# Optimization experiments

Measured on AMD Instinct MI355X. Metric: run time of the kernel, lower is better.

The kernel has to match this reference:

```python
import jax, jax.numpy as jnp
import numpy as np

# Fixed production-scale dims (equal-size graphs -> no ragged padding needed)
B, NPG, C, H, L, FFN, NC = 16, 512, 128, 8, 4, 512, 4
D = C // H          # head dim = 16
T = NPG + 1         # +1 virtual graph token
EPG = 8192          # edges per graph (avg degree 16)
E = B * EPG


def _ln(x, g, b, eps=1e-5):
    m = x.mean(-1, keepdims=True)
    v = ((x - m) ** 2).mean(-1, keepdims=True)
    return (x - m) * jax.lax.rsqrt(v + eps) * g + b


def setup_inputs() -> dict:
    key = jax.random.key(0)
    ks = jax.random.split(key, 24)
    N = B * NPG
    node_feats = jax.random.normal(ks[0], (N, 3), jnp.float32)
    # intra-graph edges: local endpoints + per-graph node offset (matches batch_ptr math)
    local = jax.random.randint(ks[1], (2, B, EPG), 0, NPG)
    offs = (jnp.arange(B) * NPG)[None, :, None]
    edge_index = (local + offs).reshape(2, E)
    edge_attr = jax.random.randint(ks[2], (E,), 0, 10)

    def nrm(k, shape, scale=0.02):
        return jax.random.normal(k, shape, jnp.float32) * scale

    params = {
        "W_node": nrm(ks[3], (3, C), 0.3), "b_node": jnp.zeros((C,), jnp.float32),
        "graph_token": nrm(ks[4], (C,), 1.0),
        "edge_bias_table": nrm(ks[5], (11, H), 0.1).at[0].set(0.0),  # padding_idx=0
        "in_deg_emb": nrm(ks[6], (512, C)).at[0].set(0.0),           # padding_idx=0
        "out_deg_emb": nrm(ks[7], (512, C)).at[0].set(0.0),
        "vnode_bias": nrm(ks[8], (H,), 1.0),
        "Wq": nrm(ks[9], (L, C, C)), "bq": jnp.zeros((L, C), jnp.float32),
        "Wk": nrm(ks[10], (L, C, C)), "bk": jnp.zeros((L, C), jnp.float32),
        "Wv": nrm(ks[11], (L, C, C)), "bv": jnp.zeros((L, C), jnp.float32),
        "Wo": nrm(ks[12], (L, C, C)), "bo": jnp.zeros((L, C), jnp.float32),
        "ln1_g": jnp.ones((L, C), jnp.float32), "ln1_b": jnp.zeros((L, C), jnp.float32),
        "ln2_g": jnp.ones((L, C), jnp.float32), "ln2_b": jnp.zeros((L, C), jnp.float32),
        "W1": nrm(ks[13], (L, C, FFN)), "b1": jnp.zeros((L, FFN), jnp.float32),
        "W2": nrm(ks[14], (L, FFN, C)), "b2": jnp.zeros((L, C), jnp.float32),
        "normf_g": jnp.ones((C,), jnp.float32), "normf_b": jnp.zeros((C,), jnp.float32),
        "Wc1": nrm(ks[15], (C, C // 2)), "bc1": jnp.zeros((C // 2,), jnp.float32),
        "Wc2": nrm(ks[16], (C // 2, NC)), "bc2": jnp.zeros((NC,), jnp.float32),
    }
    return {"node_feats": node_feats, "edge_index": edge_index,
            "edge_attr": edge_attr, "num_graphs": B, **params}


def reference(node_feats, W_node, b_node, graph_token, edge_bias_table,
              in_deg_emb, out_deg_emb, vnode_bias,
              Wq, bq, Wk, bk, Wv, bv, Wo, bo,
              ln1_g, ln1_b, ln2_g, ln2_b, W1, b1, W2, b2,
              normf_g, normf_b, Wc1, bc1, Wc2, bc2,
              edge_index, edge_attr, num_graphs):
    N = node_feats.shape[0]
    npg = N // num_graphs
    t = npg + 1
    src, dst = edge_index[0], edge_index[1]
    # degree encoders (scatter_add of ones == segment_sum)
    in_deg = jnp.clip(jax.ops.segment_sum(jnp.ones_like(dst), dst, num_segments=N), 0, 511)
    out_deg = jnp.clip(jax.ops.segment_sum(jnp.ones_like(src), src, num_segments=N), 0, 511)
    x_enc = node_feats @ W_node + b_node + in_deg_emb[in_deg] + out_deg_emb[out_deg]
    # equal-size graphs with sorted batch ids -> padding loop is a reshape, mask all-False
    x = jnp.concatenate(
        [jnp.broadcast_to(graph_token, (num_graphs, 1, C)),
         x_enc.reshape(num_graphs, npg, C)], axis=1)  # [B, T, C]
    # attention bias: vnode row/col + scattered edge-attr embeddings
    bias = jnp.zeros((num_graphs, H, t, t), jnp.float32)
    bias = bias.at[:, :, 0, :].set(vnode_bias[None, :, None])
    bias = bias.at[:, :, :, 0].set(vnode_bias[None, :, None])
    eb = edge_bias_table[jnp.clip(edge_attr, 0, 9) + 1]  # [E, H]
    g = src // npg
    sl = src - g * npg + 1
    dl = dst - g * npg + 1
    bias = bias.at[g, :, sl, dl].add(eb)  # duplicate edges accumulate (scatter_add)
    scale = 1.0 / np.sqrt(D).astype(np.float32)
    for l in range(L):  # key_padding_mask is all-False here -> masked_fill is a no-op
        h = _ln(x, ln1_g[l], ln1_b[l])
        q = (h @ Wq[l] + bq[l]).reshape(num_graphs, t, H, D)
        k = (h @ Wk[l] + bk[l]).reshape(num_graphs, t, H, D)
        v = (h @ Wv[l] + bv[l]).reshape(num_graphs, t, H, D)
        scores = jnp.einsum('bthd,bshd->bhts', q, k) * scale + bias
        attn = jax.nn.softmax(scores, axis=-1)
        o = jnp.einsum('bhts,bshd->bthd', attn, v).reshape(num_graphs, t, C)
        x = x + o @ Wo[l] + bo[l]
        h2 = _ln(x, ln2_g[l], ln2_b[l])
        x = x + jax.nn.gelu(h2 @ W1[l] + b1[l], approximate=False) @ W2[l] + b2[l]
    x = _ln(x, normf_g, normf_b)
    gr = x[:, 0, :]  # virtual-node readout
    return jax.nn.gelu(gr @ Wc1 + bc1, approximate=False) @ Wc2 + bc2
```

## Files before the change

kernel.cpp:

```cpp
#include <hip/hip_runtime.h>
#include <hip/hip_bf16.h>

#define BB 16
#define NPG 512
#define CC 128
#define HH 8
#define LL 4
#define FFN 512
#define NCLS 4
#define DD 16
#define TT 513
#define EE 131072
#define NNODES 8192
#define ROWS (BB * TT)
#define ECAP 64
#define SP 544
#define BSTR 292

static constexpr size_t XROWS = (size_t)BB * TT;
static constexpr size_t XSZ   = XROWS * CC;
static constexpr size_t VTSZ  = (size_t)BB * HH * DD * SP;

typedef unsigned short ushort_t;
typedef __attribute__((ext_vector_type(8))) short short8;
typedef __attribute__((ext_vector_type(4))) float floatx4;

__device__ __forceinline__ float gelu_exact(float v) {
    return 0.5f * v * (1.0f + erff(v * 0.70710678118654752440f));
}
__device__ __forceinline__ ushort_t f2bf(float f) {
    union { float f; unsigned u; } c; c.f = f;
    unsigned u = c.u;
    return (ushort_t)((u + 0x7FFFu + ((u >> 16) & 1u)) >> 16);
}
__device__ __forceinline__ int swz(int row, int col, int stride) {
    int kb = col >> 3;
    return row * stride + (((kb ^ (row & 7)) << 3) | (col & 7));
}

__device__ __forceinline__ void qkv_stage(const ushort_t* hs,
                                          const ushort_t* Wtq, const float* bq_,
                                          const ushort_t* Wtk, const float* bk_,
                                          const ushort_t* Wtv, const float* bv_,
                                          ushort_t* qb, ushort_t* kb, ushort_t* vt,
                                          int m0, int wave, int lq, int quad) {
    const short* hsS = (const short*)hs;
    int n0 = wave * 32;
    int c0 = n0 + lq, c1 = n0 + 16 + lq;
    const short* Ws[3] = {(const short*)Wtq, (const short*)Wtk, (const short*)Wtv};
    const float* bs[3] = {bq_, bk_, bv_};
    size_t rB0 = (size_t)(n0 + lq) * CC, rB1 = (size_t)(n0 + 16 + lq) * CC;

    #pragma unroll
    for (int m = 0; m < 3; ++m) {
        const short* W = Ws[m];
        floatx4 a0 = {0.f,0.f,0.f,0.f}, a1 = a0;
        #pragma unroll
        for (int k0 = 0; k0 < CC; k0 += 32) {
            short8 af = *(const short8*)(hsS + swz(lq, k0 + quad * 8, 128));
            short8 b0 = *(const short8*)(W + rB0 + k0 + quad * 8);
            short8 b1 = *(const short8*)(W + rB1 + k0 + quad * 8);
            a0 = __builtin_amdgcn_mfma_f32_16x16x32_bf16(af, b0, a0, 0, 0, 0);
            a1 = __builtin_amdgcn_mfma_f32_16x16x32_bf16(af, b1, a1, 0, 0, 0);
        }
        float bv0 = bs[m][c0], bv1 = bs[m][c1];
        #pragma unroll
        for (int rg = 0; rg < 4; ++rg) {
            int r = m0 + quad * 4 + rg;
            float v0 = a0[rg] + bv0;
            float v1 = a1[rg] + bv1;
            if (m == 0) {
                qb[(size_t)r * CC + c0] = f2bf(v0 * 0.25f);
                qb[(size_t)r * CC + c1] = f2bf(v1 * 0.25f);
            } else if (m == 1) {
                kb[(size_t)r * CC + c0] = f2bf(v0);
                kb[(size_t)r * CC + c1] = f2bf(v1);
            } else {
                int bg = r / TT;
                int s = r - bg * TT;
                vt[((size_t)(bg * HH + (c0 >> 4)) * DD + (c0 & 15)) * SP + s] = f2bf(v0);
                vt[((size_t)(bg * HH + (c1 >> 4)) * DD + (c1 & 15)) * SP + s] = f2bf(v1);
            }
        }
    }
}

__global__ __launch_bounds__(256) void deg_csr_kernel(const int* __restrict__ ei,
                                                      const int* __restrict__ ea,
                                                      int* __restrict__ deg_in,
                                                      int* __restrict__ deg_out,
                                                      int* __restrict__ cnt,
                                                      int* __restrict__ ebuf) {
    int e = blockIdx.x * 256 + threadIdx.x;
    if (e >= EE) return;
    int src = ei[e], dst = ei[EE + e];
    atomicAdd(&deg_out[src], 1);
    atomicAdd(&deg_in[dst], 1);
    int g = src >> 9;
    int sl = src - (g << 9) + 1;
    int dl = dst - (g << 9) + 1;
    int a = ea[e];
    a = (a < 0) ? 0 : (a > 9 ? 9 : a);
    a += 1;
    int row = g * TT + sl;
    int pos = atomicAdd(&cnt[row], 1);
    if (pos < ECAP) ebuf[(size_t)row * ECAP + pos] = dl | (a << 16);
}

__global__ __launch_bounds__(256) void encode_kernel(const float* __restrict__ nf,
                                                     const float* __restrict__ Wn,
                                                     const float* __restrict__ bn,
                                                     const float* __restrict__ gt,
                                                     const float* __restrict__ ide,
                                                     const float* __restrict__ ode,
                                                     const int* __restrict__ deg_in,
                                                     const int* __restrict__ deg_out,
                                                     float* __restrict__ x) {
    int gid = blockIdx.x * 256 + threadIdx.x;
    if (gid >= (int)(XROWS * CC)) return;
    int c = gid & (CC - 1);
    int row = gid >> 7;
    int b = row / TT;
    int t = row - b * TT;
    float val;
    if (t == 0) {
        val = gt[c];
    } else {
        int i = b * NPG + t - 1;
        val = bn[c] + nf[i*3+0]*Wn[0*CC + c] + nf[i*3+1]*Wn[1*CC + c] + nf[i*3+2]*Wn[2*CC + c];
        int di = min(deg_in[i], 511);
        int dq = min(deg_out[i], 511);
        val += ide[(size_t)di * CC + c] + ode[(size_t)dq * CC + c];
    }
    x[(size_t)row * CC + c] = val;
}

struct TrDesc {
    const float* src[24];
    ushort_t*    dst[24];
    int          K[24];
    int          N[24];
};
__global__ __launch_bounds__(256) void tr_kernel(TrDesc d) {
    int z = blockIdx.z;
    int K = d.K[z], N = d.N[z];
    int tilesN = N >> 6;
    int ntile = (K >> 6) * tilesN;
    int tile = blockIdx.x;
    if (tile >= ntile) return;
    int k0 = (tile / tilesN) << 6;
    int n0 = (tile - (tile / tilesN) * tilesN) << 6;
    const float* src = d.src[z];
    ushort_t* dst = d.dst[z];
    __shared__ float t[64][65];
    int tid = threadIdx.x;
    int c = tid & 63, rb = tid >> 6;
    #pragma unroll
    for (int kk = 0; kk < 64; kk += 4)
        t[kk + rb][c] = src[(size_t)(k0 + kk + rb) * N + n0 + c];
    __syncthreads();
    #pragma unroll
    for (int nn = 0; nn < 64; nn += 4)
        dst[(size_t)(n0 + nn + rb) * K + k0 + c] = f2bf(t[c][nn + rb]);
}

__global__ __launch_bounds__(256) void pre_kernel(const float* __restrict__ x_,
                                                  const float* __restrict__ ln1g_,
                                                  const float* __restrict__ ln1b_,
                                                  const ushort_t* __restrict__ Wtq,
                                                  const float* __restrict__ bq_,
                                                  const ushort_t* __restrict__ Wtk,
                                                  const float* __restrict__ bk_,
                                                  const ushort_t* __restrict__ Wtv,
                                                  const float* __restrict__ bv_,
                                                  ushort_t* __restrict__ qb,
                                                  ushort_t* __restrict__ kb,
                                                  ushort_t* __restrict__ vt) {
    int m0 = blockIdx.x * 16;
    int tid = threadIdx.x;
    int wave = tid >> 6, lane = tid & 63, lq = lane & 15, quad = lane >> 4;

    __shared__ ushort_t hs[16 * 128];
    __shared__ float sred[4][16][2];

    int n0 = wave * 32;
    int c0 = n0 + lq, c1 = n0 + 16 + lq;
    float w0[4], w1[4];
    #pragma unroll
    for (int rg = 0; rg < 4; ++rg) {
        int r = m0 + quad * 4 + rg;
        w0[rg] = x_[(size_t)r * CC + c0];
        w1[rg] = x_[(size_t)r * CC + c1];
    }
    #pragma unroll
    for (int rg = 0; rg < 4; ++rg) {
        float s1 = w0[rg] + w1[rg];
        float s2 = w0[rg]*w0[rg] + w1[rg]*w1[rg];
        #pragma unroll
        for (int m = 1; m < 16; m <<= 1) {
            s1 += __shfl_xor(s1, m, 64);
            s2 += __shfl_xor(s2, m, 64);
        }
        if (lq == 0) { sred[wave][quad*4+rg][0] = s1; sred[wave][quad*4+rg][1] = s2; }
    }
    __syncthreads();
    float g0 = ln1g_[c0], g1 = ln1g_[c1], lb0 = ln1b_[c0], lb1 = ln1b_[c1];
    #pragma unroll
    for (int rg = 0; rg < 4; ++rg) {
        int row = quad * 4 + rg;
        float S1 = sred[0][row][0] + sred[1][row][0] + sred[2][row][0] + sred[3][row][0];
        float S2 = sred[0][row][1] + sred[1][row][1] + sred[2][row][1] + sred[3][row][1];
        float mn = S1 * (1.0f/CC);
        float var = S2 * (1.0f/CC) - mn * mn;
        float rs = rsqrtf(var + 1e-5f);
        hs[swz(row, c0, 128)] = f2bf((w0[rg] - mn) * rs * g0 + lb0);
        hs[swz(row, c1, 128)] = f2bf((w1[rg] - mn) * rs * g1 + lb1);
    }
    __syncthreads();
    qkv_stage(hs, Wtq, bq_, Wtk, bk_, Wtv, bv_, qb, kb, vt, m0, wave, lq, quad);
}

__global__ __launch_bounds__(256) void mega_kernel(const ushort_t* __restrict__ obf,
                                                   const ushort_t* __restrict__ WtO,
                                                   const float* __restrict__ bo_,
                                                   const float* __restrict__ ln2g_,
                                                   const float* __restrict__ ln2b_,
                                                   const ushort_t* __restrict__ Wt1_,
                                                   const float* __restrict__ b1_,
                                                   const ushort_t* __restrict__ Wt2_,
                                                   const float* __restrict__ b2_,
                                                   const float* __restrict__ ln1g_,
                                                   const float* __restrict__ ln1b_,
                                                   const ushort_t* __restrict__ Wtq,
                                                   const float* __restrict__ bq_,
                                                   const ushort_t* __restrict__ Wtk,
                                                   const float* __restrict__ bk_,
                                                   const ushort_t* __restrict__ Wtv,
                                                   const float* __restrict__ bv_,
                                                   float* __restrict__ x_,
                                                   ushort_t* __restrict__ qb,
                                                   ushort_t* __restrict__ kb,
                                                   ushort_t* __restrict__ vt,
                                                   int doQKV) {
    int m0 = blockIdx.x * 16;
    int tid = threadIdx.x;
    int wave = tid >> 6, lane = tid & 63, lq = lane & 15, quad = lane >> 4;

    __shared__ ushort_t hs[16 * 128];
    __shared__ ushort_t ms[16 * 512];
    __shared__ float sred[4][16][2];

    int n0 = wave * 32;
    int c0 = n0 + lq, c1 = n0 + 16 + lq;
    float vv0[4], vv1[4];

    {
        const short* Ab = (const short*)obf;
        const short* W = (const short*)WtO;
        size_t rowA = (size_t)(m0 + lq) * CC;
        size_t rB0 = (size_t)(n0 + lq) * CC, rB1 = (size_t)(n0 + 16 + lq) * CC;
        floatx4 a0 = {0.f,0.f,0.f,0.f}, a1 = a0;
        #pragma unroll
        for (int k0 = 0; k0 < CC; k0 += 32) {
            short8 af = *(const short8*)(Ab + rowA + k0 + quad * 8);
            short8 b0 = *(const short8*)(W + rB0 + k0 + quad * 8);
            short8 b1 = *(const short8*)(W + rB1 + k0 + quad * 8);
            a0 = __builtin_amdgcn_mfma_f32_16x16x32_bf16(af, b0, a0, 0, 0, 0);
            a1 = __builtin_amdgcn_mfma_f32_16x16x32_bf16(af, b1, a1, 0, 0, 0);
        }
        float bv0 = bo_[c0], bv1 = bo_[c1];
        #pragma unroll
        for (int rg = 0; rg < 4; ++rg) {
            int r = m0 + quad * 4 + rg;
            vv0[rg] = a0[rg] + bv0 + x_[(size_t)r * CC + c0];
            vv1[rg] = a1[rg] + bv1 + x_[(size_t)r * CC + c1];
        }
        #pragma unroll
        for (int rg = 0; rg < 4; ++rg) {
            float s1 = vv0[rg] + vv1[rg];
            float s2 = vv0[rg]*vv0[rg] + vv1[rg]*vv1[rg];
            #pragma unroll
            for (int m = 1; m < 16; m <<= 1) {
                s1 += __shfl_xor(s1, m, 64);
                s2 += __shfl_xor(s2, m, 64);
            }
            if (lq == 0) { sred[wave][quad*4+rg][0] = s1; sred[wave][quad*4+rg][1] = s2; }
        }
        __syncthreads();
        float g0 = ln2g_[c0], g1 = ln2g_[c1], lb0 = ln2b_[c0], lb1 = ln2b_[c1];
        #pragma unroll
        for (int rg = 0; rg < 4; ++rg) {
            int row = quad * 4 + rg;
            float S1 = sred[0][row][0] + sred[1][row][0] + sred[2][row][0] + sred[3][row][0];
            float S2 = sred[0][row][1] + sred[1][row][1] + sred[2][row][1] + sred[3][row][1];
            float mn = S1 * (1.0f/CC);
            float var = S2 * (1.0f/CC) - mn * mn;
            float rs = rsqrtf(var + 1e-5f);
            hs[swz(row, c0, 128)] = f2bf((vv0[rg] - mn) * rs * g0 + lb0);
            hs[swz(row, c1, 128)] = f2bf((vv1[rg] - mn) * rs * g1 + lb1);
        }
    }
    __syncthreads();

    {
        const short* hsS = (const short*)hs;
        const short* W = (const short*)Wt1_;
        #pragma unroll
        for (int nt = 0; nt < 4; ++nt) {
            int n = wave * 128 + nt * 32;
            size_t rB0 = (size_t)(n + lq) * CC, rB1 = (size_t)(n + 16 + lq) * CC;
            floatx4 a0 = {0.f,0.f,0.f,0.f}, a1 = a0;
            #pragma unroll
            for (int k0 = 0; k0 < CC; k0 += 32) {
                short8 af = *(const short8*)(hsS + swz(lq, k0 + quad * 8, 128));
                short8 b0 = *(const short8*)(W + rB0 + k0 + quad * 8);
                short8 b1 = *(const short8*)(W + rB1 + k0 + quad * 8);
                a0 = __builtin_amdgcn_mfma_f32_16x16x32_bf16(af, b0, a0, 0, 0, 0);
                a1 = __builtin_amdgcn_mfma_f32_16x16x32_bf16(af, b1, a1, 0, 0, 0);
            }
            float bb0 = b1_[n + lq], bb1 = b1_[n + 16 + lq];
            #pragma unroll
            for (int rg = 0; rg < 4; ++rg) {
                int row = quad * 4 + rg;
                ms[swz(row, n + lq, 512)]      = f2bf(gelu_exact(a0[rg] + bb0));
                ms[swz(row, n + 16 + lq, 512)] = f2bf(gelu_exact(a1[rg] + bb1));
            }
        }
    }
    __syncthreads();

    {
        const short* msS = (const short*)ms;
        const short* W = (const short*)Wt2_;
        size_t rB0 = (size_t)(n0 + lq) * FFN, rB1 = (size_t)(n0 + 16 + lq) * FFN;
        floatx4 a0 = {0.f,0.f,0.f,0.f}, a1 = a0;
        #pragma unroll 4
        for (int k0 = 0; k0 < FFN; k0 += 32) {
            short8 af = *(const short8*)(msS + swz(lq, k0 + quad * 8, 512));
            short8 b0 = *(const short8*)(W + rB0 + k0 + quad * 8);
            short8 b1 = *(const short8*)(W + rB1 + k0 + quad * 8);
            a0 = __builtin_amdgcn_mfma_f32_16x16x32_bf16(af, b0, a0, 0, 0, 0);
            a1 = __builtin_amdgcn_mfma_f32_16x16x32_bf16(af, b1, a1, 0, 0, 0);
        }
        float bv0 = b2_[c0], bv1 = b2_[c1];
        float w0[4], w1[4];
        #pragma unroll
        for (int rg = 0; rg < 4; ++rg) {
            int r = m0 + quad * 4 + rg;
            w0[rg] = a0[rg] + bv0 + vv0[rg];
            w1[rg] = a1[rg] + bv1 + vv1[rg];
            x_[(size_t)r * CC + c0] = w0[rg];
            x_[(size_t)r * CC + c1] = w1[rg];
        }
        if (!doQKV) return;
        #pragma unroll
        for (int rg = 0; rg < 4; ++rg) {
            float s1 = w0[rg] + w1[rg];
            float s2 = w0[rg]*w0[rg] + w1[rg]*w1[rg];
            #pragma unroll
            for (int m = 1; m < 16; m <<= 1) {
                s1 += __shfl_xor(s1, m, 64);
                s2 += __shfl_xor(s2, m, 64);
            }
            if (lq == 0) { sred[wave][quad*4+rg][0] = s1; sred[wave][quad*4+rg][1] = s2; }
        }
        __syncthreads();
        float g0 = ln1g_[c0], g1 = ln1g_[c1], lb0 = ln1b_[c0], lb1 = ln1b_[c1];
        #pragma unroll
        for (int rg = 0; rg < 4; ++rg) {
            int row = quad * 4 + rg;
            float S1 = sred[0][row][0] + sred[1][row][0] + sred[2][row][0] + sred[3][row][0];
            float S2 = sred[0][row][1] + sred[1][row][1] + sred[2][row][1] + sred[3][row][1];
            float mn = S1 * (1.0f/CC);
            float var = S2 * (1.0f/CC) - mn * mn;
            float rs = rsqrtf(var + 1e-5f);
            hs[swz(row, c0, 128)] = f2bf((w0[rg] - mn) * rs * g0 + lb0);
            hs[swz(row, c1, 128)] = f2bf((w1[rg] - mn) * rs * g1 + lb1);
        }
    }
    __syncthreads();

    qkv_stage(hs, Wtq, bq_, Wtk, bk_, Wtv, bv_, qb, kb, vt, m0, wave, lq, quad);
}

__global__ __launch_bounds__(256) void attn_kernel(const ushort_t* __restrict__ qb,
                                                   const ushort_t* __restrict__ kb,
                                                   const ushort_t* __restrict__ vt,
                                                   const int* __restrict__ cnt,
                                                   const int* __restrict__ ebuf,
                                                   const float* __restrict__ ebt,
                                                   const float* __restrict__ vnode,
                                                   ushort_t* __restrict__ ob) {
    int bh = blockIdx.x;
    int qt = blockIdx.y;
    int b = bh >> 3, h = bh & (HH - 1);
    int tid = threadIdx.x;
    int wave = tid >> 6, lane = tid & 63, lq = lane & 15, quad = lane >> 4;

    __shared__ float arena[16 * BSTR];
    float* bstrip = arena;

    int qg = qt * 16 + lq;
    int qr = qg < TT ? qg : TT - 1;
    short8 qf = {0,0,0,0,0,0,0,0};
    if (quad < 2)
        qf = *(const short8*)(qb + ((size_t)(b * TT + qr)) * CC + h * DD + quad * 8);
    float vbh = vnode[h];
    int ql = tid >> 4, e0 = tid & 15;
    int qs = qt * 16 + ql;
    int crow = b * TT + (qs < TT ? qs : 0);
    int cn = (qs > 0 && qs < TT) ? min(cnt[crow], ECAP) : 0;

    const short* kbS = (const short*)kb;
    const short* vtS = (const short*)(vt + (size_t)bh * DD * SP);

    floatx4 oacc = {0.f, 0.f, 0.f, 0.f};
    float lsum = 0.f;

    #pragma unroll
    for (int ch = 0; ch < 2; ++ch) {
        int sp_lo = ch ? 9 : 0;
        int sp_hi = ch ? 17 : 9;
        int s_lo  = ch ? 288 : 0;
        int nrows = ch ? 256 : 288;

        int sp = sp_lo + wave;
        short8 af0 = {0,0,0,0,0,0,0,0}, af1 = af0, vf = af0;
        if (sp < sp_hi) {
            int st0 = sp * 2, st1 = sp * 2 + 1;
            int kr0 = min(b * TT + st0 * 16 + lq, (int)XROWS - 1);
            int kr1 = min(b * TT + st1 * 16 + lq, (int)XROWS - 1);
            if (quad < 2) {
                af0 = *(const short8*)(kbS + (size_t)kr0 * CC + h * DD + quad * 8);
                af1 = *(const short8*)(kbS + (size_t)kr1 * CC + h * DD + quad * 8);
            }
            vf = *(const short8*)(vtS + (size_t)lq * SP + sp * 32 + quad * 8);
        }

        for (int i = tid; i < 16 * BSTR / 4; i += 256)
            ((float4*)bstrip)[i] = make_float4(0.f, 0.f, 0.f, 0.f);
        __syncthreads();
        if (ch == 0 && tid < 16) {
            int q = qt * 16 + tid;
            if (q > 0 && q < TT) bstrip[tid * BSTR] = vbh;
        }
        for (int j = e0; j < cn; j += 16) {
            int e = ebuf[(size_t)crow * ECAP + j];
            int dl = e & 0xFFFF, a = e >> 16;
            int loc = dl - s_lo;
            if (loc >= 0 && loc < nrows)
                atomicAdd(&bstrip[ql * BSTR + loc], ebt[a * 8 + h]);
        }
        __syncthreads();

        for (; sp < sp_hi; sp += 4) {
            int spn = sp + 4;
            short8 nf0 = {0,0,0,0,0,0,0,0}, nf1 = nf0, nvf = nf0;
            if (spn < sp_hi) {
                int st0 = spn * 2, st1 = spn * 2 + 1;
                int kr0 = min(b * TT + st0 * 16 + lq, (int)XROWS - 1);
                int kr1 = min(b * TT + st1 * 16 + lq, (int)XROWS - 1);
                if (quad < 2) {
                    nf0 = *(const short8*)(kbS + (size_t)kr0 * CC + h * DD + quad * 8);
                    nf1 = *(const short8*)(kbS + (size_t)kr1 * CC + h * DD + quad * 8);
                }
                nvf = *(const short8*)(vtS + (size_t)lq * SP + spn * 32 + quad * 8);
            }

            unsigned pw[2][2];
            #pragma unroll
            for (int t = 0; t < 2; ++t) {
                int st = sp * 2 + t;
                floatx4 c = __builtin_amdgcn_mfma_f32_16x16x32_bf16(
                    t ? af1 : af0, qf, (floatx4){0.f, 0.f, 0.f, 0.f}, 0, 0, 0);
                float4 bi = *(const float4*)(bstrip + lq * BSTR + (st * 16 - s_lo) + quad * 4);
                float biv[4] = {bi.x, bi.y, bi.z, bi.w};
                float pr[4];
                #pragma unroll
                for (int rg = 0; rg < 4; ++rg) {
                    int s = st * 16 + quad * 4 + rg;
                    float p = 0.f;
                    if (s < TT) p = __expf(c[rg] + biv[rg]);
                    lsum += p;
                    pr[rg] = p;
                }
                pw[t][0] = (unsigned)f2bf(pr[0]) | ((unsigned)f2bf(pr[1]) << 16);
                pw[t][1] = (unsigned)f2bf(pr[2]) | ((unsigned)f2bf(pr[3]) << 16);
            }
            int srcA = lq + (((2 * quad) & 3) << 4);
            int srcB = lq + (((2 * quad + 1) & 3) << 4);
            int a00 = __shfl((int)pw[0][0], srcA, 64);
            int a01 = __shfl((int)pw[0][1], srcA, 64);
            int a10 = __shfl((int)pw[1][0], srcA, 64);
            int a11 = __shfl((int)pw[1][1], srcA, 64);
            int b00 = __shfl((int)pw[0][0], srcB, 64);
            int b01 = __shfl((int)pw[0][1], srcB, 64);
            int b10 = __shfl((int)pw[1][0], srcB, 64);
            int b11 = __shfl((int)pw[1][1], srcB, 64);
            union { int u[4]; short8 s8; } pu;
            bool lo = quad < 2;
            pu.u[0] = lo ? a00 : a10;
            pu.u[1] = lo ? a01 : a11;
            pu.u[2] = lo ? b00 : b10;
            pu.u[3] = lo ? b01 : b11;
            oacc = __builtin_amdgcn_mfma_f32_16x16x32_bf16(vf, pu.s8, oacc, 0, 0, 0);

            af0 = nf0; af1 = nf1; vf = nvf;
        }
        __syncthreads();
    }

    lsum += __shfl_xor(lsum, 16, 64);
    lsum += __shfl_xor(lsum, 32, 64);
    float* redw = arena;
    float* lsumS = arena + 1088;
    #pragma unroll
    for (int rg = 0; rg < 4; ++rg)
        redw[wave * 272 + (quad * 4 + rg) * 17 + lq] = oacc[rg];
    if (quad == 0) lsumS[wave * 16 + lq] = lsum;
    __syncthreads();

    {
        int q = tid >> 4, d = tid & 15;
        float o = 0.f, L = 0.f;
        #pragma unroll
        for (int w = 0; w < 4; ++w) {
            o += redw[w * 272 + d * 17 + q];
            L += lsumS[w * 16 + q];
        }
        int qq = qt * 16 + q;
        if (qq < TT)
            ob[((size_t)(b * TT + qq)) * CC + h * DD + d] = f2bf(o / L);
    }
}

__global__ __launch_bounds__(128) void head_kernel(const float* __restrict__ x,
                                                   const float* __restrict__ ng,
                                                   const float* __restrict__ nb,
                                                   const float* __restrict__ Wc1,
                                                   const float* __restrict__ bc1,
                                                   const float* __restrict__ Wc2,
                                                   const float* __restrict__ bc2,
                                                   float* __restrict__ out) {
    int b = blockIdx.x;
    int c = threadIdx.x;
    __shared__ float xfs[CC];
    __shared__ float c1s[64];
    __shared__ float red[4];

    float v = x[((size_t)b * TT) * CC + c];
    float s1 = v, s2 = v * v;
    #pragma unroll
    for (int m = 32; m >= 1; m >>= 1) {
        s1 += __shfl_xor(s1, m, 64);
        s2 += __shfl_xor(s2, m, 64);
    }
    int w = c >> 6;
    if ((c & 63) == 0) { red[w*2] = s1; red[w*2+1] = s2; }
    __syncthreads();
    float S1 = red[0] + red[2], S2 = red[1] + red[3];
    float mn = S1 * (1.0f/CC);
    float var = S2 * (1.0f/CC) - mn * mn;
    float rs = rsqrtf(var + 1e-5f);
    xfs[c] = (v - mn) * rs * ng[c] + nb[c];
    __syncthreads();
    if (c < 64) {
        float a = bc1[c];
        #pragma unroll 4
        for (int k = 0; k < CC; ++k) a = fmaf(xfs[k], Wc1[(size_t)k * 64 + c], a);
        c1s[c] = gelu_exact(a);
    }
    __syncthreads();
    if (c < NCLS) {
        float a = bc2[c];
        #pragma unroll 4
        for (int j = 0; j < 64; ++j) a = fmaf(c1s[j], Wc2[(size_t)j * NCLS + c], a);
        out[(size_t)b * NCLS + c] = a;
    }
}

extern "C" void kernel_launch(void* const* d_in, const int* in_sizes, int n_in,
                              void* d_out, int out_size, void* d_ws, size_t ws_size,
                              hipStream_t stream) {
    const float* node_feats = (const float*)d_in[0];
    const int*   edge_index = (const int*)d_in[1];
    const int*   edge_attr  = (const int*)d_in[2];
    const float* W_node  = (const float*)d_in[4];
    const float* b_node  = (const float*)d_in[5];
    const float* g_token = (const float*)d_in[6];
    const float* ebt     = (const float*)d_in[7];
    const float* ide     = (const float*)d_in[8];
    const float* ode     = (const float*)d_in[9];
    const float* vnode   = (const float*)d_in[10];
    const float* Wq = (const float*)d_in[11];
    const float* bq = (const float*)d_in[12];
    const float* Wk = (const float*)d_in[13];
    const float* bk = (const float*)d_in[14];
    const float* Wv = (const float*)d_in[15];
    const float* bv = (const float*)d_in[16];
    const float* Wo = (const float*)d_in[17];
    const float* bo = (const float*)d_in[18];
    const float* ln1g = (const float*)d_in[19];
    const float* ln1b = (const float*)d_in[20];
    const float* ln2g = (const float*)d_in[21];
    const float* ln2b = (const float*)d_in[22];
    const float* W1 = (const float*)d_in[23];
    const float* b1 = (const float*)d_in[24];
    const float* W2 = (const float*)d_in[25];
    const float* b2 = (const float*)d_in[26];
    const float* nfg = (const float*)d_in[27];
    const float* nfb = (const float*)d_in[28];
    const float* Wc1 = (const float*)d_in[29];
    const float* bc1 = (const float*)d_in[30];
    const float* Wc2 = (const float*)d_in[31];
    const float* bc2 = (const float*)d_in[32];
    float* out = (float*)d_out;

    char* base = (char*)d_ws;
    float* x      = (float*)base;     base += XSZ * 4;
    ushort_t* qb  = (ushort_t*)base;  base += XSZ * 2;
    ushort_t* kb  = (ushort_t*)base;  base += XSZ * 2;
    ushort_t* vt  = (ushort_t*)base;  base += VTSZ * 2;
    ushort_t* obf = (ushort_t*)base;  base += XSZ * 2;
    ushort_t* wtqkvo = (ushort_t*)base; base += (size_t)16 * 16384 * 2;
    ushort_t* wt1 = (ushort_t*)base;  base += (size_t)4 * 65536 * 2;
    ushort_t* wt2 = (ushort_t*)base;  base += (size_t)4 * 65536 * 2;
    int* deg_in  = (int*)base;        base += NNODES * 4;
    int* deg_out = (int*)base;        base += NNODES * 4;
    int* cnt     = (int*)base;        base += (size_t)ROWS * 4;
    int* ebuf    = (int*)base;        base += (size_t)ROWS * ECAP * 4;

    hipMemsetAsync(deg_in, 0, (size_t)(2 * NNODES + ROWS) * 4, stream);
    deg_csr_kernel<<<EE / 256, 256, 0, stream>>>(edge_index, edge_attr,
                                                 deg_in, deg_out, cnt, ebuf);
    encode_kernel<<<(int)((XROWS * CC + 255) / 256), 256, 0, stream>>>(
        node_feats, W_node, b_node, g_token, ide, ode, deg_in, deg_out, x);

    TrDesc td;
    for (int l = 0; l < LL; ++l) {
        const float* srcs[4] = {Wq + (size_t)l*CC*CC, Wk + (size_t)l*CC*CC,
                                Wv + (size_t)l*CC*CC, Wo + (size_t)l*CC*CC};
        for (int k = 0; k < 4; ++k) {
            int slot = k * 4 + l;
            td.src[slot] = srcs[k];
            td.dst[slot] = wtqkvo + (size_t)slot * 16384;
            td.K[slot] = CC; td.N[slot] = CC;
        }
        td.src[16 + l] = W1 + (size_t)l*CC*FFN;
        td.dst[16 + l] = wt1 + (size_t)l*65536;
        td.K[16 + l] = CC; td.N[16 + l] = FFN;
        td.src[20 + l] = W2 + (size_t)l*FFN*CC;
        td.dst[20 + l] = wt2 + (size_t)l*65536;
        td.K[20 + l] = FFN; td.N[20 + l] = CC;
    }
    tr_kernel<<<dim3(16, 1, 24), 256, 0, stream>>>(td);

    const int MT16 = (int)(XROWS / 16);

    pre_kernel<<<MT16, 256, 0, stream>>>(
        x, ln1g, ln1b,
        wtqkvo + (size_t)(0*4+0)*16384, bq,
        wtqkvo + (size_t)(1*4+0)*16384, bk,
        wtqkvo + (size_t)(2*4+0)*16384, bv,
        qb, kb, vt);

    for (int l = 0; l < LL; ++l) {
        attn_kernel<<<dim3(BB*HH, 33), 256, 0, stream>>>(
            qb, kb, vt, cnt, ebuf, ebt, vnode, obf);

        int ln = (l + 1) % LL;
        mega_kernel<<<MT16, 256, 0, stream>>>(
            obf,
            wtqkvo + (size_t)(3*4+l)*16384, bo + l*CC,
            ln2g + l*CC, ln2b + l*CC,
            wt1 + (size_t)l*65536, b1 + l*FFN,
            wt2 + (size_t)l*65536, b2 + l*CC,
            ln1g + ln*CC, ln1b + ln*CC,
            wtqkvo + (size_t)(0*4+ln)*16384, bq + ln*CC,
            wtqkvo + (size_t)(1*4+ln)*16384, bk + ln*CC,
            wtqkvo + (size_t)(2*4+ln)*16384, bv + ln*CC,
            x, qb, kb, vt,
            (l < LL-1) ? 1 : 0);
    }

    head_kernel<<<BB, 128, 0, stream>>>(x, nfg, nfb, Wc1, bc1, Wc2, bc2, out);
}
```

Measured before the change: 436.0 us.

## Fuse all stages into one persistent cooperative kernel with grid syncs

Replaces the chain of separate kernel launches (degree/CSR build, encode, weight transpose, QKV, per-layer attention and MLP, head) with a single persistent cooperative kernel. Blocks loop over the work of each phase and separate phases with grid-wide syncs. The aim is to remove per-launch overhead and launch gaps. In exchange, the number of resident blocks is capped by occupancy, a shared-memory arena is reused across phases, and grid syncs add their own cost. A multi-launch fallback is kept for when cooperative launch is unavailable.

```diff
diff --git a/kernel.cpp b/kernel.cpp
--- a/kernel.cpp
+++ b/kernel.cpp
@@ -1,5 +1,8 @@
 #include <hip/hip_runtime.h>
 #include <hip/hip_bf16.h>
+#include <hip/hip_cooperative_groups.h>
+
+namespace cg = cooperative_groups;
 
 #define BB 16
 #define NPG 512
@@ -16,6 +19,7 @@
 #define ECAP 64
 #define SP 544
 #define BSTR 292
+#define MT16 513
 
 static constexpr size_t XROWS = (size_t)BB * TT;
 static constexpr size_t XSZ   = XROWS * CC;
@@ -24,6 +28,17 @@
 typedef unsigned short ushort_t;
 typedef __attribute__((ext_vector_type(8))) short short8;
 typedef __attribute__((ext_vector_type(4))) float floatx4;
+
+struct KArgs {
+    const float *node_feats, *W_node, *b_node, *g_token, *ebt, *ide, *ode, *vnode;
+    const float *Wq, *bq, *Wk, *bk, *Wv, *bv, *Wo, *bo;
+    const float *ln1g, *ln1b, *ln2g, *ln2b;
+    const float *W1, *b1, *W2, *b2, *nfg, *nfb, *Wc1, *bc1, *Wc2, *bc2;
+    const int *edge_index, *edge_attr;
+    float *x, *out;
+    ushort_t *qb, *kb, *vt, *obf, *wtqkvo, *wt1, *wt2;
+    int *deg_in, *deg_out, *cnt, *ebuf;
+};
 
 __device__ __forceinline__ float gelu_exact(float v) {
     return 0.5f * v * (1.0f + erff(v * 0.70710678118654752440f));
@@ -38,12 +53,11 @@
     return row * stride + (((kb ^ (row & 7)) << 3) | (col & 7));
 }
 
-__device__ __forceinline__ void qkv_stage(const ushort_t* hs,
-                                          const ushort_t* Wtq, const float* bq_,
-                                          const ushort_t* Wtk, const float* bk_,
-                                          const ushort_t* Wtv, const float* bv_,
-                                          ushort_t* qb, ushort_t* kb, ushort_t* vt,
-                                          int m0, int wave, int lq, int quad) {
+__device__ __forceinline__ void qkv_stage4(const KArgs& a, const ushort_t* hs,
+                                           const ushort_t* Wtq, const float* bq_,
+                                           const ushort_t* Wtk, const float* bk_,
+                                           const ushort_t* Wtv, const float* bv_,
+                                           int m0, int wave, int lq, int quad) {
     const short* hsS = (const short*)hs;
     int n0 = wave * 32;
     int c0 = n0 + lq, c1 = n0 + 16 + lq;
@@ -70,349 +84,39 @@
             float v0 = a0[rg] + bv0;
             float v1 = a1[rg] + bv1;
             if (m == 0) {
-                qb[(size_t)r * CC + c0] = f2bf(v0 * 0.25f);
-                qb[(size_t)r * CC + c1] = f2bf(v1 * 0.25f);
+                a.qb[(size_t)r * CC + c0] = f2bf(v0 * 0.25f);
+                a.qb[(size_t)r * CC + c1] = f2bf(v1 * 0.25f);
             } else if (m == 1) {
-                kb[(size_t)r * CC + c0] = f2bf(v0);
-                kb[(size_t)r * CC + c1] = f2bf(v1);
+                a.kb[(size_t)r * CC + c0] = f2bf(v0);
+                a.kb[(size_t)r * CC + c1] = f2bf(v1);
             } else {
                 int bg = r / TT;
                 int s = r - bg * TT;
-                vt[((size_t)(bg * HH + (c0 >> 4)) * DD + (c0 & 15)) * SP + s] = f2bf(v0);
-                vt[((size_t)(bg * HH + (c1 >> 4)) * DD + (c1 & 15)) * SP + s] = f2bf(v1);
-            }
-        }
-    }
-}
-
-__global__ __launch_bounds__(256) void deg_csr_kernel(const int* __restrict__ ei,
-                                                      const int* __restrict__ ea,
-                                                      int* __restrict__ deg_in,
-                                                      int* __restrict__ deg_out,
-                                                      int* __restrict__ cnt,
-                                                      int* __restrict__ ebuf) {
-    int e = blockIdx.x * 256 + threadIdx.x;
-    if (e >= EE) return;
-    int src = ei[e], dst = ei[EE + e];
-    atomicAdd(&deg_out[src], 1);
-    atomicAdd(&deg_in[dst], 1);
-    int g = src >> 9;
-    int sl = src - (g << 9) + 1;
-    int dl = dst - (g << 9) + 1;
-    int a = ea[e];
-    a = (a < 0) ? 0 : (a > 9 ? 9 : a);
-    a += 1;
-    int row = g * TT + sl;
-    int pos = atomicAdd(&cnt[row], 1);
-    if (pos < ECAP) ebuf[(size_t)row * ECAP + pos] = dl | (a << 16);
-}
-
-__global__ __launch_bounds__(256) void encode_kernel(const float* __restrict__ nf,
-                                                     const float* __restrict__ Wn,
-                                                     const float* __restrict__ bn,
-                                                     const float* __restrict__ gt,
-                                                     const float* __restrict__ ide,
-                                                     const float* __restrict__ ode,
-                                                     const int* __restrict__ deg_in,
-                                                     const int* __restrict__ deg_out,
-                                                     float* __restrict__ x) {
-    int gid = blockIdx.x * 256 + threadIdx.x;
-    if (gid >= (int)(XROWS * CC)) return;
-    int c = gid & (CC - 1);
-    int row = gid >> 7;
-    int b = row / TT;
-    int t = row - b * TT;
-    float val;
-    if (t == 0) {
-        val = gt[c];
-    } else {
-        int i = b * NPG + t - 1;
-        val = bn[c] + nf[i*3+0]*Wn[0*CC + c] + nf[i*3+1]*Wn[1*CC + c] + nf[i*3+2]*Wn[2*CC + c];
-        int di = min(deg_in[i], 511);
-        int dq = min(deg_out[i], 511);
-        val += ide[(size_t)di * CC + c] + ode[(size_t)dq * CC + c];
-    }
-    x[(size_t)row * CC + c] = val;
-}
-
-struct TrDesc {
-    const float* src[24];
-    ushort_t*    dst[24];
-    int          K[24];
-    int          N[24];
-};
-__global__ __launch_bounds__(256) void tr_kernel(TrDesc d) {
-    int z = blockIdx.z;
-    int K = d.K[z], N = d.N[z];
-    int tilesN = N >> 6;
-    int ntile = (K >> 6) * tilesN;
-    int tile = blockIdx.x;
-    if (tile >= ntile) return;
-    int k0 = (tile / tilesN) << 6;
-    int n0 = (tile - (tile / tilesN) * tilesN) << 6;
-    const float* src = d.src[z];
-    ushort_t* dst = d.dst[z];
-    __shared__ float t[64][65];
-    int tid = threadIdx.x;
-    int c = tid & 63, rb = tid >> 6;
-    #pragma unroll
-    for (int kk = 0; kk < 64; kk += 4)
-        t[kk + rb][c] = src[(size_t)(k0 + kk + rb) * N + n0 + c];
-    __syncthreads();
-    #pragma unroll
-    for (int nn = 0; nn < 64; nn += 4)
-        dst[(size_t)(n0 + nn + rb) * K + k0 + c] = f2bf(t[c][nn + rb]);
-}
-
-__global__ __launch_bounds__(256) void pre_kernel(const float* __restrict__ x_,
-                                                  const float* __restrict__ ln1g_,
-                                                  const float* __restrict__ ln1b_,
-                                                  const ushort_t* __restrict__ Wtq,
-                                                  const float* __restrict__ bq_,
-                                                  const ushort_t* __restrict__ Wtk,
-                                                  const float* __restrict__ bk_,
-                                                  const ushort_t* __restrict__ Wtv,
-                                                  const float* __restrict__ bv_,
-                                                  ushort_t* __restrict__ qb,
-                                                  ushort_t* __restrict__ kb,
-                                                  ushort_t* __restrict__ vt) {
-    int m0 = blockIdx.x * 16;
-    int tid = threadIdx.x;
+                a.vt[((size_t)(bg * HH + (c0 >> 4)) * DD + (c0 & 15)) * SP + s] = f2bf(v0);
+                a.vt[((size_t)(bg * HH + (c1 >> 4)) * DD + (c1 & 15)) * SP + s] = f2bf(v1);
+            }
+        }
+    }
+}
+
+__device__ void attn_tile(const KArgs& a, char* arena, int bh, int qt, int tid) {
+    int b = bh >> 3, h = bh & (HH - 1);
     int wave = tid >> 6, lane = tid & 63, lq = lane & 15, quad = lane >> 4;
-
-    __shared__ ushort_t hs[16 * 128];
-    __shared__ float sred[4][16][2];
-
-    int n0 = wave * 32;
-    int c0 = n0 + lq, c1 = n0 + 16 + lq;
-    float w0[4], w1[4];
-    #pragma unroll
-    for (int rg = 0; rg < 4; ++rg) {
-        int r = m0 + quad * 4 + rg;
-        w0[rg] = x_[(size_t)r * CC + c0];
-        w1[rg] = x_[(size_t)r * CC + c1];
-    }
-    #pragma unroll
-    for (int rg = 0; rg < 4; ++rg) {
-        float s1 = w0[rg] + w1[rg];
-        float s2 = w0[rg]*w0[rg] + w1[rg]*w1[rg];
-        #pragma unroll
-        for (int m = 1; m < 16; m <<= 1) {
-            s1 += __shfl_xor(s1, m, 64);
-            s2 += __shfl_xor(s2, m, 64);
-        }
-        if (lq == 0) { sred[wave][quad*4+rg][0] = s1; sred[wave][quad*4+rg][1] = s2; }
-    }
-    __syncthreads();
-    float g0 = ln1g_[c0], g1 = ln1g_[c1], lb0 = ln1b_[c0], lb1 = ln1b_[c1];
-    #pragma unroll
-    for (int rg = 0; rg < 4; ++rg) {
-        int row = quad * 4 + rg;
-        float S1 = sred[0][row][0] + sred[1][row][0] + sred[2][row][0] + sred[3][row][0];
-        float S2 = sred[0][row][1] + sred[1][row][1] + sred[2][row][1] + sred[3][row][1];
-        float mn = S1 * (1.0f/CC);
-        float var = S2 * (1.0f/CC) - mn * mn;
-        float rs = rsqrtf(var + 1e-5f);
-        hs[swz(row, c0, 128)] = f2bf((w0[rg] - mn) * rs * g0 + lb0);
-        hs[swz(row, c1, 128)] = f2bf((w1[rg] - mn) * rs * g1 + lb1);
-    }
-    __syncthreads();
-    qkv_stage(hs, Wtq, bq_, Wtk, bk_, Wtv, bv_, qb, kb, vt, m0, wave, lq, quad);
-}
-
-__global__ __launch_bounds__(256) void mega_kernel(const ushort_t* __restrict__ obf,
-                                                   const ushort_t* __restrict__ WtO,
-                                                   const float* __restrict__ bo_,
-                                                   const float* __restrict__ ln2g_,
-                                                   const float* __restrict__ ln2b_,
-                                                   const ushort_t* __restrict__ Wt1_,
-                                                   const float* __restrict__ b1_,
-                                                   const ushort_t* __restrict__ Wt2_,
-                                                   const float* __restrict__ b2_,
-                                                   const float* __restrict__ ln1g_,
-                                                   const float* __restrict__ ln1b_,
-                                                   const ushort_t* __restrict__ Wtq,
-                                                   const float* __restrict__ bq_,
-                                                   const ushort_t* __restrict__ Wtk,
-                                                   const float* __restrict__ bk_,
-                                                   const ushort_t* __restrict__ Wtv,
-                                                   const float* __restrict__ bv_,
-                                                   float* __restrict__ x_,
-                                                   ushort_t* __restrict__ qb,
-                                                   ushort_t* __restrict__ kb,
-                                                   ushort_t* __restrict__ vt,
-                                                   int doQKV) {
-    int m0 = blockIdx.x * 16;
-    int tid = threadIdx.x;
-    int wave = tid >> 6, lane = tid & 63, lq = lane & 15, quad = lane >> 4;
-
-    __shared__ ushort_t hs[16 * 128];
-    __shared__ ushort_t ms[16 * 512];
-    __shared__ float sred[4][16][2];
-
-    int n0 = wave * 32;
-    int c0 = n0 + lq, c1 = n0 + 16 + lq;
-    float vv0[4], vv1[4];
-
-    {
-        const short* Ab = (const short*)obf;
-        const short* W = (const short*)WtO;
-        size_t rowA = (size_t)(m0 + lq) * CC;
-        size_t rB0 = (size_t)(n0 + lq) * CC, rB1 = (size_t)(n0 + 16 + lq) * CC;
-        floatx4 a0 = {0.f,0.f,0.f,0.f}, a1 = a0;
-        #pragma unroll
-        for (int k0 = 0; k0 < CC; k0 += 32) {
-            short8 af = *(const short8*)(Ab + rowA + k0 + quad * 8);
-            short8 b0 = *(const short8*)(W + rB0 + k0 + quad * 8);
-            short8 b1 = *(const short8*)(W + rB1 + k0 + quad * 8);
-            a0 = __builtin_amdgcn_mfma_f32_16x16x32_bf16(af, b0, a0, 0, 0, 0);
-            a1 = __builtin_amdgcn_mfma_f32_16x16x32_bf16(af, b1, a1, 0, 0, 0);
-        }
-        float bv0 = bo_[c0], bv1 = bo_[c1];
-        #pragma unroll
-        for (int rg = 0; rg < 4; ++rg) {
-            int r = m0 + quad * 4 + rg;
-            vv0[rg] = a0[rg] + bv0 + x_[(size_t)r * CC + c0];
-            vv1[rg] = a1[rg] + bv1 + x_[(size_t)r * CC + c1];
-        }
-        #pragma unroll
-        for (int rg = 0; rg < 4; ++rg) {
-            float s1 = vv0[rg] + vv1[rg];
-            float s2 = vv0[rg]*vv0[rg] + vv1[rg]*vv1[rg];
-            #pragma unroll
-            for (int m = 1; m < 16; m <<= 1) {
-                s1 += __shfl_xor(s1, m, 64);
-                s2 += __shfl_xor(s2, m, 64);
-            }
-            if (lq == 0) { sred[wave][quad*4+rg][0] = s1; sred[wave][quad*4+rg][1] = s2; }
-        }
-        __syncthreads();
-        float g0 = ln2g_[c0], g1 = ln2g_[c1], lb0 = ln2b_[c0], lb1 = ln2b_[c1];
-        #pragma unroll
-        for (int rg = 0; rg < 4; ++rg) {
-            int row = quad * 4 + rg;
-            float S1 = sred[0][row][0] + sred[1][row][0] + sred[2][row][0] + sred[3][row][0];
-            float S2 = sred[0][row][1] + sred[1][row][1] + sred[2][row][1] + sred[3][row][1];
-            float mn = S1 * (1.0f/CC);
-            float var = S2 * (1.0f/CC) - mn * mn;
-            float rs = rsqrtf(var + 1e-5f);
-            hs[swz(row, c0, 128)] = f2bf((vv0[rg] - mn) * rs * g0 + lb0);
-            hs[swz(row, c1, 128)] = f2bf((vv1[rg] - mn) * rs * g1 + lb1);
-        }
-    }
-    __syncthreads();
-
-    {
-        const short* hsS = (const short*)hs;
-        const short* W = (const short*)Wt1_;
-        #pragma unroll
-        for (int nt = 0; nt < 4; ++nt) {
-            int n = wave * 128 + nt * 32;
-            size_t rB0 = (size_t)(n + lq) * CC, rB1 = (size_t)(n + 16 + lq) * CC;
-            floatx4 a0 = {0.f,0.f,0.f,0.f}, a1 = a0;
-            #pragma unroll
-            for (int k0 = 0; k0 < CC; k0 += 32) {
-                short8 af = *(const short8*)(hsS + swz(lq, k0 + quad * 8, 128));
-                short8 b0 = *(const short8*)(W + rB0 + k0 + quad * 8);
-                short8 b1 = *(const short8*)(W + rB1 + k0 + quad * 8);
-                a0 = __builtin_amdgcn_mfma_f32_16x16x32_bf16(af, b0, a0, 0, 0, 0);
-                a1 = __builtin_amdgcn_mfma_f32_16x16x32_bf16(af, b1, a1, 0, 0, 0);
-            }
-            float bb0 = b1_[n + lq], bb1 = b1_[n + 16 + lq];
-            #pragma unroll
-            for (int rg = 0; rg < 4; ++rg) {
-                int row = quad * 4 + rg;
-                ms[swz(row, n + lq, 512)]      = f2bf(gelu_exact(a0[rg] + bb0));
-                ms[swz(row, n + 16 + lq, 512)] = f2bf(gelu_exact(a1[rg] + bb1));
-            }
-        }
-    }
-    __syncthreads();
-
-    {
-        const short* msS = (const short*)ms;
-        const short* W = (const short*)Wt2_;
-        size_t rB0 = (size_t)(n0 + lq) * FFN, rB1 = (size_t)(n0 + 16 + lq) * FFN;
-        floatx4 a0 = {0.f,0.f,0.f,0.f}, a1 = a0;
-        #pragma unroll 4
-        for (int k0 = 0; k0 < FFN; k0 += 32) {
-            short8 af = *(const short8*)(msS + swz(lq, k0 + quad * 8, 512));
-            short8 b0 = *(const short8*)(W + rB0 + k0 + quad * 8);
-            short8 b1 = *(const short8*)(W + rB1 + k0 + quad * 8);
-            a0 = __builtin_amdgcn_mfma_f32_16x16x32_bf16(af, b0, a0, 0, 0, 0);
-            a1 = __builtin_amdgcn_mfma_f32_16x16x32_bf16(af, b1, a1, 0, 0, 0);
-        }
-        float bv0 = b2_[c0], bv1 = b2_[c1];
-        float w0[4], w1[4];
-        #pragma unroll
-        for (int rg = 0; rg < 4; ++rg) {
-            int r = m0 + quad * 4 + rg;
-            w0[rg] = a0[rg] + bv0 + vv0[rg];
-            w1[rg] = a1[rg] + bv1 + vv1[rg];
-            x_[(size_t)r * CC + c0] = w0[rg];
-            x_[(size_t)r * CC + c1] = w1[rg];
-        }
-        if (!doQKV) return;
-        #pragma unroll
-        for (int rg = 0; rg < 4; ++rg) {
-            float s1 = w0[rg] + w1[rg];
-            float s2 = w0[rg]*w0[rg] + w1[rg]*w1[rg];
-            #pragma unroll
-            for (int m = 1; m < 16; m <<= 1) {
-                s1 += __shfl_xor(s1, m, 64);
-                s2 += __shfl_xor(s2, m, 64);
-            }
-            if (lq == 0) { sred[wave][quad*4+rg][0] = s1; sred[wave][quad*4+rg][1] = s2; }
-        }
-        __syncthreads();
-        float g0 = ln1g_[c0], g1 = ln1g_[c1], lb0 = ln1b_[c0], lb1 = ln1b_[c1];
-        #pragma unroll
-        for (int rg = 0; rg < 4; ++rg) {
-            int row = quad * 4 + rg;
-            float S1 = sred[0][row][0] + sred[1][row][0] + sred[2][row][0] + sred[3][row][0];
-            float S2 = sred[0][row][1] + sred[1][row][1] + sred[2][row][1] + sred[3][row][1];
-            float mn = S1 * (1.0f/CC);
-            float var = S2 * (1.0f/CC) - mn * mn;
-            float rs = rsqrtf(var + 1e-5f);
-            hs[swz(row, c0, 128)] = f2bf((w0[rg] - mn) * rs * g0 + lb0);
-            hs[swz(row, c1, 128)] = f2bf((w1[rg] - mn) * rs * g1 + lb1);
-        }
-    }
-    __syncthreads();
-
-    qkv_stage(hs, Wtq, bq_, Wtk, bk_, Wtv, bv_, qb, kb, vt, m0, wave, lq, quad);
-}
-
-__global__ __launch_bounds__(256) void attn_kernel(const ushort_t* __restrict__ qb,
-                                                   const ushort_t* __restrict__ kb,
-                                                   const ushort_t* __restrict__ vt,
-                                                   const int* __restrict__ cnt,
-                                                   const int* __restrict__ ebuf,
-                                                   const float* __restrict__ ebt,
-                                                   const float* __restrict__ vnode,
-                                                   ushort_t* __restrict__ ob) {
-    int bh = blockIdx.x;
-    int qt = blockIdx.y;
-    int b = bh >> 3, h = bh & (HH - 1);
-    int tid = threadIdx.x;
-    int wave = tid >> 6, lane = tid & 63, lq = lane & 15, quad = lane >> 4;
-
-    __shared__ float arena[16 * BSTR];
-    float* bstrip = arena;
+    float* bstrip = (float*)arena;
 
     int qg = qt * 16 + lq;
     int qr = qg < TT ? qg : TT - 1;
     short8 qf = {0,0,0,0,0,0,0,0};
     if (quad < 2)
-        qf = *(const short8*)(qb + ((size_t)(b * TT + qr)) * CC + h * DD + quad * 8);
-    float vbh = vnode[h];
+        qf = *(const short8*)(a.qb + ((size_t)(b * TT + qr)) * CC + h * DD + quad * 8);
+    float vbh = a.vnode[h];
     int ql = tid >> 4, e0 = tid & 15;
     int qs = qt * 16 + ql;
     int crow = b * TT + (qs < TT ? qs : 0);
-    int cn = (qs > 0 && qs < TT) ? min(cnt[crow], ECAP) : 0;
-
-    const short* kbS = (const short*)kb;
-    const short* vtS = (const short*)(vt + (size_t)bh * DD * SP);
+    int cn = (qs > 0 && qs < TT) ? min(a.cnt[crow], ECAP) : 0;
+
+    const short* kbS = (const short*)a.kb;
+    const short* vtS = (const short*)(a.vt + (size_t)bh * DD * SP);
 
     floatx4 oacc = {0.f, 0.f, 0.f, 0.f};
     float lsum = 0.f;
@@ -445,11 +149,11 @@
             if (q > 0 && q < TT) bstrip[tid * BSTR] = vbh;
         }
         for (int j = e0; j < cn; j += 16) {
-            int e = ebuf[(size_t)crow * ECAP + j];
-            int dl = e & 0xFFFF, a = e >> 16;
+            int e = a.ebuf[(size_t)crow * ECAP + j];
+            int dl = e & 0xFFFF, aa = e >> 16;
             int loc = dl - s_lo;
             if (loc >= 0 && loc < nrows)
-                atomicAdd(&bstrip[ql * BSTR + loc], ebt[a * 8 + h]);
+                atomicAdd(&bstrip[ql * BSTR + loc], a.ebt[aa * 8 + h]);
         }
         __syncthreads();
 
@@ -512,8 +216,8 @@
 
     lsum += __shfl_xor(lsum, 16, 64);
     lsum += __shfl_xor(lsum, 32, 64);
-    float* redw = arena;
-    float* lsumS = arena + 1088;
+    float* redw = (float*)arena;
+    float* lsumS = (float*)arena + 1088;
     #pragma unroll
     for (int rg = 0; rg < 4; ++rg)
         redw[wave * 272 + (quad * 4 + rg) * 17 + lq] = oacc[rg];
@@ -530,158 +234,456 @@
         }
         int qq = qt * 16 + q;
         if (qq < TT)
-            ob[((size_t)(b * TT + qq)) * CC + h * DD + d] = f2bf(o / L);
-    }
-}
-
-__global__ __launch_bounds__(128) void head_kernel(const float* __restrict__ x,
-                                                   const float* __restrict__ ng,
-                                                   const float* __restrict__ nb,
-                                                   const float* __restrict__ Wc1,
-                                                   const float* __restrict__ bc1,
-                                                   const float* __restrict__ Wc2,
-                                                   const float* __restrict__ bc2,
-                                                   float* __restrict__ out) {
-    int b = blockIdx.x;
-    int c = threadIdx.x;
-    __shared__ float xfs[CC];
-    __shared__ float c1s[64];
-    __shared__ float red[4];
-
-    float v = x[((size_t)b * TT) * CC + c];
-    float s1 = v, s2 = v * v;
+            a.obf[((size_t)(b * TT + qq)) * CC + h * DD + d] = f2bf(o / L);
+    }
+    __syncthreads();
+}
+
+__device__ void mega_tile(const KArgs& a, char* arena, int l, int m0, int tid, int doQKV) {
+    int wave = tid >> 6, lane = tid & 63, lq = lane & 15, quad = lane >> 4;
+    ushort_t* hs = (ushort_t*)arena;
+    ushort_t* ms = (ushort_t*)(arena + 4096);
+    float* sred = (float*)(arena + 20480);
+
+    const ushort_t* WtO = a.wtqkvo + (size_t)(12 + l) * 16384;
+    const float* bo_ = a.bo + l * CC;
+    const float* ln2g_ = a.ln2g + l * CC;
+    const float* ln2b_ = a.ln2b + l * CC;
+    const ushort_t* Wt1_ = a.wt1 + (size_t)l * 65536;
+    const float* b1_ = a.b1 + l * FFN;
+    const ushort_t* Wt2_ = a.wt2 + (size_t)l * 65536;
+    const float* b2_ = a.b2 + l * CC;
+    int ln = (l + 1) % LL;
+    const float* ln1g_ = a.ln1g + ln * CC;
+    const float* ln1b_ = a.ln1b + ln * CC;
+
+    int n0 = wave * 32;
+    int c0 = n0 + lq, c1 = n0 + 16 + lq;
+    float vv0[4], vv1[4];
+
+    {
+        const short* Ab = (const short*)a.obf;
+        const short* W = (const short*)WtO;
+        size_t rowA = (size_t)(m0 + lq) * CC;
+        size_t rB0 = (size_t)(n0 + lq) * CC, rB1 = (size_t)(n0 + 16 + lq) * CC;
+        floatx4 a0 = {0.f,0.f,0.f,0.f}, a1 = a0;
+        #pragma unroll
+        for (int k0 = 0; k0 < CC; k0 += 32) {
+            short8 af = *(const short8*)(Ab + rowA + k0 + quad * 8);
+            short8 b0 = *(const short8*)(W + rB0 + k0 + quad * 8);
+            short8 b1 = *(const short8*)(W + rB1 + k0 + quad * 8);
+            a0 = __builtin_amdgcn_mfma_f32_16x16x32_bf16(af, b0, a0, 0, 0, 0);
+            a1 = __builtin_amdgcn_mfma_f32_16x16x32_bf16(af, b1, a1, 0, 0, 0);
+        }
+        float bv0 = bo_[c0], bv1 = bo_[c1];
+        #pragma unroll
+        for (int rg = 0; rg < 4; ++rg) {
+            int r = m0 + quad * 4 + rg;
+            vv0[rg] = a0[rg] + bv0 + a.x[(size_t)r * CC + c0];
+            vv1[rg] = a1[rg] + bv1 + a.x[(size_t)r * CC + c1];
+        }
+        #pragma unroll
+        for (int rg = 0; rg < 4; ++rg) {
+            float s1 = vv0[rg] + vv1[rg];
+            float s2 = vv0[rg]*vv0[rg] + vv1[rg]*vv1[rg];
+            #pragma unroll
+            for (int m = 1; m < 16; m <<= 1) {
+                s1 += __shfl_xor(s1, m, 64);
+                s2 += __shfl_xor(s2, m, 64);
+            }
+            if (lq == 0) { sred[(wave*16 + quad*4+rg)*2+0] = s1; sred[(wave*16 + quad*4+rg)*2+1] = s2; }
+        }
+        __syncthreads();
+        float g0 = ln2g_[c0], g1 = ln2g_[c1], lb0 = ln2b_[c0], lb1 = ln2b_[c1];
+        #pragma unroll
+        for (int rg = 0; rg < 4; ++rg) {
+            int row = quad * 4 + rg;
+            float S1 = 0.f, S2 = 0.f;
+            #pragma unroll
+            for (int w = 0; w < 4; ++w) { S1 += sred[(w*16+row)*2+0]; S2 += sred[(w*16+row)*2+1]; }
+            float mn = S1 * (1.0f/CC);
+            float var = S2 * (1.0f/CC) - mn * mn;
+            float rs = rsqrtf(var + 1e-5f);
+            hs[swz(row, c0, 128)] = f2bf((vv0[rg] - mn) * rs * g0 + lb0);
+            hs[swz(row, c1, 128)] = f2bf((vv1[rg] - mn) * rs * g1 + lb1);
+        }
+    }
+    __syncthreads();
+
+    {
+        const short* hsS = (const short*)hs;
+        const short* W = (const short*)Wt1_;
+        #pragma unroll
+        for (int nt = 0; nt < 4; ++nt) {
+            int n = wave * 128 + nt * 32;
+            size_t rB0 = (size_t)(n + lq) * CC, rB1 = (size_t)(n + 16 + lq) * CC;
+            floatx4 a0 = {0.f,0.f,0.f,0.f}, a1 = a0;
+            #pragma unroll
+            for (int k0 = 0; k0 < CC; k0 += 32) {
+                short8 af = *(const short8*)(hsS + swz(lq, k0 + quad * 8, 128));
+                short8 b0 = *(const short8*)(W + rB0 + k0 + quad * 8);
+                short8 b1 = *(const short8*)(W + rB1 + k0 + quad * 8);
+                a0 = __builtin_amdgcn_mfma_f32_16x16x32_bf16(af, b0, a0, 0, 0, 0);
+                a1 = __builtin_amdgcn_mfma_f32_16x16x32_bf16(af, b1, a1, 0, 0, 0);
+            }
+            float bb0 = b1_[n + lq], bb1 = b1_[n + 16 + lq];
+            #pragma unroll
+            for (int rg = 0; rg < 4; ++rg) {
+                int row = quad * 4 + rg;
+                ms[swz(row, n + lq, 512)]      = f2bf(gelu_exact(a0[rg] + bb0));
+                ms[swz(row, n + 16 + lq, 512)] = f2bf(gelu_exact(a1[rg] + bb1));
+            }
+        }
+    }
+    __syncthreads();
+
+    {
+        const short* msS = (const short*)ms;
+        const short* W = (const short*)Wt2_;
+        size_t rB0 = (size_t)(n0 + lq) * FFN, rB1 = (size_t)(n0 + 16 + lq) * FFN;
+        floatx4 a0 = {0.f,0.f,0.f,0.f}, a1 = a0;
+        #pragma unroll 4
+        for (int k0 = 0; k0 < FFN; k0 += 32) {
+            short8 af = *(const short8*)(msS + swz(lq, k0 + quad * 8, 512));
+            short8 b0 = *(const short8*)(W + rB0 + k0 + quad * 8);
+            short8 b1 = *(const short8*)(W + rB1 + k0 + quad * 8);
+            a0 = __builtin_amdgcn_mfma_f32_16x16x32_bf16(af, b0, a0, 0, 0, 0);
+            a1 = __builtin_amdgcn_mfma_f32_16x16x32_bf16(af, b1, a1, 0, 0, 0);
+        }
+        float bv0 = b2_[c0], bv1 = b2_[c1];
+        float w0[4], w1[4];
+        #pragma unroll
+        for (int rg = 0; rg < 4; ++rg) {
+            int r = m0 + quad * 4 + rg;
+            w0[rg] = a0[rg] + bv0 + vv0[rg];
+            w1[rg] = a1[rg] + bv1 + vv1[rg];
+            a.x[(size_t)r * CC + c0] = w0[rg];
+            a.x[(size_t)r * CC + c1] = w1[rg];
+        }
+        if (doQKV) {
+            #pragma unroll
+            for (int rg = 0; rg < 4; ++rg) {
+                float s1 = w0[rg] + w1[rg];
+                float s2 = w0[rg]*w0[rg] + w1[rg]*w1[rg];
+                #pragma unroll
+                for (int m = 1; m < 16; m <<= 1) {
+                    s1 += __shfl_xor(s1, m, 64);
+                    s2 += __shfl_xor(s2, m, 64);
+                }
+                if (lq == 0) { sred[(wave*16 + quad*4+rg)*2+0] = s1; sred[(wave*16 + quad*4+rg)*2+1] = s2; }
+            }
+            __syncthreads();
+            float g0 = ln1g_[c0], g1 = ln1g_[c1], lb0 = ln1b_[c0], lb1 = ln1b_[c1];
+            #pragma unroll
+            for (int rg = 0; rg < 4; ++rg) {
+                int row = quad * 4 + rg;
+                float S1 = 0.f, S2 = 0.f;
+                #pragma unroll
+                for (int w = 0; w < 4; ++w) { S1 += sred[(w*16+row)*2+0]; S2 += sred[(w*16+row)*2+1]; }
+                float mn = S1 * (1.0f/CC);
+                float var = S2 * (1.0f/CC) - mn * mn;
+                float rs = rsqrtf(var + 1e-5f);
+                hs[swz(row, c0, 128)] = f2bf((w0[rg] - mn) * rs * g0 + lb0);
+                hs[swz(row, c1, 128)] = f2bf((w1[rg] - mn) * rs * g1 + lb1);
+            }
+        }
+    }
+    if (doQKV) {
+        __syncthreads();
+        qkv_stage4(a, hs,
+                   a.wtqkvo + (size_t)(0 + ln) * 16384, a.bq + ln * CC,
+                   a.wtqkvo + (size_t)(4 + ln) * 16384, a.bk + ln * CC,
+                   a.wtqkvo + (size_t)(8 + ln) * 16384, a.bv + ln * CC,
+                   m0, wave, lq, quad);
+    }
+}
+
+__device__ void pre_tile(const KArgs& a, char* arena, int m0, int tid) {
+    int wave = tid >> 6, lane = tid & 63, lq = lane & 15, quad = lane >> 4;
+    ushort_t* hs = (ushort_t*)arena;
+    float* sred = (float*)(arena + 20480);
+
+    int n0 = wave * 32;
+    int c0 = n0 + lq, c1 = n0 + 16 + lq;
+    float w0[4], w1[4];
+    #pragma unroll
+    for (int rg = 0; rg < 4; ++rg) {
+        int r = m0 + quad * 4 + rg;
+        w0[rg] = a.x[(size_t)r * CC + c0];
+        w1[rg] = a.x[(size_t)r * CC + c1];
+    }
+    #pragma unroll
+    for (int rg = 0; rg < 4; ++rg) {
+        float s1 = w0[rg] + w1[rg];
+        float s2 = w0[rg]*w0[rg] + w1[rg]*w1[rg];
+        #pragma unroll
+        for (int m = 1; m < 16; m <<= 1) {
+            s1 += __shfl_xor(s1, m, 64);
+            s2 += __shfl_xor(s2, m, 64);
+        }
+        if (lq == 0) { sred[(wave*16 + quad*4+rg)*2+0] = s1; sred[(wave*16 + quad*4+rg)*2+1] = s2; }
+    }
+    __syncthreads();
+    float g0 = a.ln1g[c0], g1 = a.ln1g[c1], lb0 = a.ln1b[c0], lb1 = a.ln1b[c1];
+    #pragma unroll
+    for (int rg = 0; rg < 4; ++rg) {
+        int row = quad * 4 + rg;
+        float S1 = 0.f, S2 = 0.f;
+        #pragma unroll
+        for (int w = 0; w < 4; ++w) { S1 += sred[(w*16+row)*2+0]; S2 += sred[(w*16+row)*2+1]; }
+        float mn = S1 * (1.0f/CC);
+        float var = S2 * (1.0f/CC) - mn * mn;
+        float rs = rsqrtf(var + 1e-5f);
+        hs[swz(row, c0, 128)] = f2bf((w0[rg] - mn) * rs * g0 + lb0);
+        hs[swz(row, c1, 128)] = f2bf((w1[rg] - mn) * rs * g1 + lb1);
+    }
+    __syncthreads();
+    qkv_stage4(a, hs, a.wtqkvo, a.bq,
+               a.wtqkvo + (size_t)4 * 16384, a.bk,
+               a.wtqkvo + (size_t)8 * 16384, a.bv,
+               m0, wave, lq, quad);
+}
+
+__device__ void tr_tile(const KArgs& a, char* arena, int z, int tid) {
+    const float* src; ushort_t* dst; int K, N, tile;
+    if (z < 64) {
+        int zz = z >> 2; tile = z & 3;
+        int k = zz >> 2, l = zz & 3;
+        const float* s4[4] = {a.Wq, a.Wk, a.Wv, a.Wo};
+        src = s4[k] + (size_t)l * CC * CC;
+        dst = a.wtqkvo + (size_t)(k * 4 + l) * 16384;
+        K = CC; N = CC;
+    } else if (z < 128) {
+        int l = (z - 64) >> 4; tile = (z - 64) & 15;
+        src = a.W1 + (size_t)l * CC * FFN;
+        dst = a.wt1 + (size_t)l * 65536;
+        K = CC; N = FFN;
+    } else {
+        int l = (z - 128) >> 4; tile = (z - 128) & 15;
+        src = a.W2 + (size_t)l * FFN * CC;
+        dst = a.wt2 + (size_t)l * 65536;
+        K = FFN; N = CC;
+    }
+    int tilesN = N >> 6;
+    int k0 = (tile / tilesN) << 6;
+    int n0 = (tile - (tile / tilesN) * tilesN) << 6;
+    float (*tt)[65] = (float(*)[65])arena;
+    int c = tid & 63, rb = tid >> 6;
+    #pragma unroll
+    for (int kk = 0; kk < 64; kk += 4)
+        tt[kk + rb][c] = src[(size_t)(k0 + kk + rb) * N + n0 + c];
+    __syncthreads();
+    #pragma unroll
+    for (int nn = 0; nn < 64; nn += 4)
+        dst[(size_t)(n0 + nn + rb) * K + k0 + c] = f2bf(tt[c][nn + rb]);
+}
+
+__device__ void head_tile(const KArgs& a, char* arena, int b, int tid) {
+    float* xfs = (float*)arena;
+    float* c1s = xfs + CC;
+    float* red = c1s + 64;
+    int c = tid;
+    float v = 0.f, s1 = 0.f, s2 = 0.f;
+    if (c < CC) {
+        v = a.x[((size_t)b * TT) * CC + c];
+        s1 = v; s2 = v * v;
+    }
     #pragma unroll
     for (int m = 32; m >= 1; m >>= 1) {
         s1 += __shfl_xor(s1, m, 64);
         s2 += __shfl_xor(s2, m, 64);
     }
     int w = c >> 6;
-    if ((c & 63) == 0) { red[w*2] = s1; red[w*2+1] = s2; }
-    __syncthreads();
-    float S1 = red[0] + red[2], S2 = red[1] + red[3];
-    float mn = S1 * (1.0f/CC);
-    float var = S2 * (1.0f/CC) - mn * mn;
-    float rs = rsqrtf(var + 1e-5f);
-    xfs[c] = (v - mn) * rs * ng[c] + nb[c];
+    if (c < CC && (c & 63) == 0) { red[w*2] = s1; red[w*2+1] = s2; }
+    __syncthreads();
+    if (c < CC) {
+        float S1 = red[0] + red[2], S2 = red[1] + red[3];
+        float mn = S1 * (1.0f/CC);
+        float var = S2 * (1.0f/CC) - mn * mn;
+        float rs = rsqrtf(var + 1e-5f);
+        xfs[c] = (v - mn) * rs * a.nfg[c] + a.nfb[c];
+    }
     __syncthreads();
     if (c < 64) {
-        float a = bc1[c];
+        float acc = a.bc1[c];
         #pragma unroll 4
-        for (int k = 0; k < CC; ++k) a = fmaf(xfs[k], Wc1[(size_t)k * 64 + c], a);
-        c1s[c] = gelu_exact(a);
+        for (int k = 0; k < CC; ++k) acc = fmaf(xfs[k], a.Wc1[(size_t)k * 64 + c], acc);
+        c1s[c] = gelu_exact(acc);
     }
     __syncthreads();
     if (c < NCLS) {
-        float a = bc2[c];
+        float acc = a.bc2[c];
         #pragma unroll 4
-        for (int j = 0; j < 64; ++j) a = fmaf(c1s[j], Wc2[(size_t)j * NCLS + c], a);
-        out[(size_t)b * NCLS + c] = a;
-    }
+        for (int j = 0; j < 64; ++j) acc = fmaf(c1s[j], a.Wc2[(size_t)j * NCLS + c], acc);
+        a.out[(size_t)b * NCLS + c] = acc;
+    }
+}
+
+__device__ void do_phase(const KArgs& a, char* arena, int phase, int l,
+                         int bid, int NB, int tid) {
+    if (phase == 0) {
+        for (int i = bid * 256 + tid; i < 2 * NNODES + ROWS; i += NB * 256)
+            a.deg_in[i] = 0;
+    } else if (phase == 1) {
+        for (int e = bid * 256 + tid; e < EE; e += NB * 256) {
+            int src = a.edge_index[e], dst = a.edge_index[EE + e];
+            atomicAdd(&a.deg_out[src], 1);
+            atomicAdd(&a.deg_in[dst], 1);
+            int g = src >> 9;
+            int sl = src - (g << 9) + 1;
+            int dl = dst - (g << 9) + 1;
+            int aa = a.edge_attr[e];
+            aa = (aa < 0) ? 0 : (aa > 9 ? 9 : aa);
+            aa += 1;
+            int row = g * TT + sl;
+            int pos = atomicAdd(&a.cnt[row], 1);
+            if (pos < ECAP) a.ebuf[(size_t)row * ECAP + pos] = dl | (aa << 16);
+        }
+    } else if (phase == 2) {
+        for (int z = bid; z < 192; z += NB) {
+            tr_tile(a, arena, z, tid);
+            __syncthreads();
+        }
+        for (int gi = bid * 256 + tid; gi < (int)(XROWS * CC); gi += NB * 256) {
+            int c = gi & (CC - 1);
+            int row = gi >> 7;
+            int b = row / TT;
+            int t = row - b * TT;
+            float val;
+            if (t == 0) {
+                val = a.g_token[c];
+            } else {
+                int i = b * NPG + t - 1;
+                val = a.b_node[c] + a.node_feats[i*3+0]*a.W_node[0*CC + c]
+                                 + a.node_feats[i*3+1]*a.W_node[1*CC + c]
+                                 + a.node_feats[i*3+2]*a.W_node[2*CC + c];
+                int di = min(a.deg_in[i], 511);
+                int dq = min(a.deg_out[i], 511);
+                val += a.ide[(size_t)di * CC + c] + a.ode[(size_t)dq * CC + c];
+            }
+            a.x[(size_t)row * CC + c] = val;
+        }
+    } else if (phase == 3) {
+        for (int t = bid; t < MT16; t += NB) {
+            pre_tile(a, arena, t * 16, tid);
+            __syncthreads();
+        }
+    } else if (phase == 4) {
+        for (int t = bid; t < BB * HH * 33; t += NB)
+            attn_tile(a, arena, t / 33, t - (t / 33) * 33, tid);
+    } else if (phase == 5) {
+        for (int t = bid; t < MT16; t += NB) {
+            mega_tile(a, arena, l, t * 16, tid, l < LL - 1);
+            __syncthreads();
+        }
+    } else {
+        for (int b = bid; b < BB; b += NB) {
+            head_tile(a, arena, b, tid);
+            __syncthreads();
+        }
+    }
+}
+
+__global__ __launch_bounds__(256) void fused_kernel(KArgs a) {
+    cg::grid_group grid = cg::this_grid();
+    __shared__ __align__(16) char arena[21504];
+    const int tid = threadIdx.x, bid = blockIdx.x, NB = gridDim.x;
+
+    do_phase(a, arena, 0, 0, bid, NB, tid); grid.sync();
+    do_phase(a, arena, 1, 0, bid, NB, tid); grid.sync();
+    do_phase(a, arena, 2, 0, bid, NB, tid); grid.sync();
+    do_phase(a, arena, 3, 0, bid, NB, tid); grid.sync();
+    for (int l = 0; l < LL; ++l) {
+        do_phase(a, arena, 4, l, bid, NB, tid); grid.sync();
+        do_phase(a, arena, 5, l, bid, NB, tid); grid.sync();
+    }
+    do_phase(a, arena, 6, 0, bid, NB, tid);
+}
+
+__global__ __launch_bounds__(256) void phase_kernel(KArgs a, int phase, int l) {
+    __shared__ __align__(16) char arena[21504];
+    do_phase(a, arena, phase, l, blockIdx.x, gridDim.x, threadIdx.x);
 }
 
 extern "C" void kernel_launch(void* const* d_in, const int* in_sizes, int n_in,
                               void* d_out, int out_size, void* d_ws, size_t ws_size,
                               hipStream_t stream) {
-    const float* node_feats = (const float*)d_in[0];
-    const int*   edge_index = (const int*)d_in[1];
-    const int*   edge_attr  = (const int*)d_in[2];
-    const float* W_node  = (const float*)d_in[4];
-    const float* b_node  = (const float*)d_in[5];
-    const float* g_token = (const float*)d_in[6];
-    const float* ebt     = (const float*)d_in[7];
-    const float* ide     = (const float*)d_in[8];
-    const float* ode     = (const float*)d_in[9];
-    const float* vnode   = (const float*)d_in[10];
-    const float* Wq = (const float*)d_in[11];
-    const float* bq = (const float*)d_in[12];
-    const float* Wk = (const float*)d_in[13];
-    const float* bk = (const float*)d_in[14];
-    const float* Wv = (const float*)d_in[15];
-    const float* bv = (const float*)d_in[16];
-    const float* Wo = (const float*)d_in[17];
-    const float* bo = (const float*)d_in[18];
-    const float* ln1g = (const float*)d_in[19];
-    const float* ln1b = (const float*)d_in[20];
-    const float* ln2g = (const float*)d_in[21];
-    const float* ln2b = (const float*)d_in[22];
-    const float* W1 = (const float*)d_in[23];
-    const float* b1 = (const float*)d_in[24];
-    const float* W2 = (const float*)d_in[25];
-    const float* b2 = (const float*)d_in[26];
-    const float* nfg = (const float*)d_in[27];
-    const float* nfb = (const float*)d_in[28];
-    const float* Wc1 = (const float*)d_in[29];
-    const float* bc1 = (const float*)d_in[30];
-    const float* Wc2 = (const float*)d_in[31];
-    const float* bc2 = (const float*)d_in[32];
-    float* out = (float*)d_out;
+    KArgs ka;
+    ka.node_feats = (const float*)d_in[0];
+    ka.edge_index = (const int*)d_in[1];
+    ka.edge_attr  = (const int*)d_in[2];
+    ka.W_node  = (const float*)d_in[4];
+    ka.b_node  = (const float*)d_in[5];
+    ka.g_token = (const float*)d_in[6];
+    ka.ebt     = (const float*)d_in[7];
+    ka.ide     = (const float*)d_in[8];
+    ka.ode     = (const float*)d_in[9];
+    ka.vnode   = (const float*)d_in[10];
+    ka.Wq = (const float*)d_in[11];
+    ka.bq = (const float*)d_in[12];
+    ka.Wk = (const float*)d_in[13];
+    ka.bk = (const float*)d_in[14];
+    ka.Wv = (const float*)d_in[15];
+    ka.bv = (const float*)d_in[16];
+    ka.Wo = (const float*)d_in[17];
+    ka.bo = (const float*)d_in[18];
+    ka.ln1g = (const float*)d_in[19];
+    ka.ln1b = (const float*)d_in[20];
+    ka.ln2g = (const float*)d_in[21];
+    ka.ln2b = (const float*)d_in[22];
+    ka.W1 = (const float*)d_in[23];
+    ka.b1 = (const float*)d_in[24];
+    ka.W2 = (const float*)d_in[25];
+    ka.b2 = (const float*)d_in[26];
+    ka.nfg = (const float*)d_in[27];
+    ka.nfb = (const float*)d_in[28];
+    ka.Wc1 = (const float*)d_in[29];
+    ka.bc1 = (const float*)d_in[30];
+    ka.Wc2 = (const float*)d_in[31];
+    ka.bc2 = (const float*)d_in[32];
+    ka.out = (float*)d_out;
 
     char* base = (char*)d_ws;
-    float* x      = (float*)base;     base += XSZ * 4;
-    ushort_t* qb  = (ushort_t*)base;  base += XSZ * 2;
-    ushort_t* kb  = (ushort_t*)base;  base += XSZ * 2;
-    ushort_t* vt  = (ushort_t*)base;  base += VTSZ * 2;
-    ushort_t* obf = (ushort_t*)base;  base += XSZ * 2;
-    ushort_t* wtqkvo = (ushort_t*)base; base += (size_t)16 * 16384 * 2;
-    ushort_t* wt1 = (ushort_t*)base;  base += (size_t)4 * 65536 * 2;
-    ushort_t* wt2 = (ushort_t*)base;  base += (size_t)4 * 65536 * 2;
-    int* deg_in  = (int*)base;        base += NNODES * 4;
-    int* deg_out = (int*)base;        base += NNODES * 4;
-    int* cnt     = (int*)base;        base += (size_t)ROWS * 4;
-    int* ebuf    = (int*)base;        base += (size_t)ROWS * ECAP * 4;
-
-    hipMemsetAsync(deg_in, 0, (size_t)(2 * NNODES + ROWS) * 4, stream);
-    deg_csr_kernel<<<EE / 256, 256, 0, stream>>>(edge_index, edge_attr,
-                                                 deg_in, deg_out, cnt, ebuf);
-    encode_kernel<<<(int)((XROWS * CC + 255) / 256), 256, 0, stream>>>(
-        node_feats, W_node, b_node, g_token, ide, ode, deg_in, deg_out, x);
-
-    TrDesc td;
-    for (int l = 0; l < LL; ++l) {
-        const float* srcs[4] = {Wq + (size_t)l*CC*CC, Wk + (size_t)l*CC*CC,
-                                Wv + (size_t)l*CC*CC, Wo + (size_t)l*CC*CC};
-        for (int k = 0; k < 4; ++k) {
-            int slot = k * 4 + l;
-            td.src[slot] = srcs[k];
-            td.dst[slot] = wtqkvo + (size_t)slot * 16384;
-            td.K[slot] = CC; td.N[slot] = CC;
-        }
-        td.src[16 + l] = W1 + (size_t)l*CC*FFN;
-        td.dst[16 + l] = wt1 + (size_t)l*65536;
-        td.K[16 + l] = CC; td.N[16 + l] = FFN;
-        td.src[20 + l] = W2 + (size_t)l*FFN*CC;
-        td.dst[20 + l] = wt2 + (size_t)l*65536;
-        td.K[20 + l] = FFN; td.N[20 + l] = CC;
-    }
-    tr_kernel<<<dim3(16, 1, 24), 256, 0, stream>>>(td);
-
-    const int MT16 = (int)(XROWS / 16);
-
-    pre_kernel<<<MT16, 256, 0, stream>>>(
-        x, ln1g, ln1b,
-        wtqkvo + (size_t)(0*4+0)*16384, bq,
-        wtqkvo + (size_t)(1*4+0)*16384, bk,
-        wtqkvo + (size_t)(2*4+0)*16384, bv,
-        qb, kb, vt);
-
-    for (int l = 0; l < LL; ++l) {
-        attn_kernel<<<dim3(BB*HH, 33), 256, 0, stream>>>(
-            qb, kb, vt, cnt, ebuf, ebt, vnode, obf);
-
-        int ln = (l + 1) % LL;
-        mega_kernel<<<MT16, 256, 0, stream>>>(
-            obf,
-            wtqkvo + (size_t)(3*4+l)*16384, bo + l*CC,
-            ln2g + l*CC, ln2b + l*CC,
-            wt1 + (size_t)l*65536, b1 + l*FFN,
-            wt2 + (size_t)l*65536, b2 + l*CC,
-            ln1g + ln*CC, ln1b + ln*CC,
-            wtqkvo + (size_t)(0*4+ln)*16384, bq + ln*CC,
-            wtqkvo + (size_t)(1*4+ln)*16384, bk + ln*CC,
-            wtqkvo + (size_t)(2*4+ln)*16384, bv + ln*CC,
-            x, qb, kb, vt,
-            (l < LL-1) ? 1 : 0);
-    }
-
-    head_kernel<<<BB, 128, 0, stream>>>(x, nfg, nfb, Wc1, bc1, Wc2, bc2, out);
-}
+    ka.x      = (float*)base;     base += XSZ * 4;
+    ka.qb     = (ushort_t*)base;  base += XSZ * 2;
+    ka.kb     = (ushort_t*)base;  base += XSZ * 2;
+    ka.vt     = (ushort_t*)base;  base += VTSZ * 2;
+    ka.obf    = (ushort_t*)base;  base += XSZ * 2;
+    ka.wtqkvo = (ushort_t*)base;  base += (size_t)16 * 16384 * 2;
+    ka.wt1    = (ushort_t*)base;  base += (size_t)4 * 65536 * 2;
+    ka.wt2    = (ushort_t*)base;  base += (size_t)4 * 65536 * 2;
+    ka.deg_in  = (int*)base;      base += NNODES * 4;
+    ka.deg_out = (int*)base;      base += NNODES * 4;
+    ka.cnt     = (int*)base;      base += (size_t)ROWS * 4;
+    ka.ebuf    = (int*)base;      base += (size_t)ROWS * ECAP * 4;
+
+    int dev = 0;
+    hipGetDevice(&dev);
+    int coopOK = 0;
+    hipDeviceGetAttribute(&coopOK, hipDeviceAttributeCooperativeLaunch, dev);
+    int ncu = 0;
+    hipDeviceGetAttribute(&ncu, hipDeviceAttributeMultiprocessorCount, dev);
+    int occ = 0;
+    hipOccupancyMaxActiveBlocksPerMultiprocessor(&occ, fused_kernel, 256, 0);
+    long nb = (long)occ * (long)ncu;
+    if (nb > 1024) nb = 1024;
+
+    hipError_t err = hipErrorUnknown;
+    if (coopOK && nb >= 64) {
+        void* params[] = { &ka };
+        err = hipLaunchCooperativeKernel(fused_kernel, dim3((unsigned)nb), dim3(256),
+                                         params, 0, stream);
+    }
+    if (err != hipSuccess) {
+        (void)hipGetLastError();
+        phase_kernel<<<97,   256, 0, stream>>>(ka, 0, 0);
+        phase_kernel<<<512,  256, 0, stream>>>(ka, 1, 0);
+        phase_kernel<<<4104, 256, 0, stream>>>(ka, 2, 0);
+        phase_kernel<<<513,  256, 0, stream>>>(ka, 3, 0);
+        for (int l = 0; l < LL; ++l) {
+            phase_kernel<<<4224, 256, 0, stream>>>(ka, 4, l);
+            phase_kernel<<<513,  256, 0, stream>>>(ka, 5, l);
+        }
+        phase_kernel<<<16, 256, 0, stream>>>(ka, 6, 0);
+    }
+}
```

Result: slower. 577.3 us (+32.4%).
